# Kernel optimization log

Measured on AMD Instinct MI355X. Metric: run time of the kernel, lower is better.

The kernel has to match this reference:

```python
import jax, jax.numpy as jnp
import numpy as np

NODE_CARDS = [119, 5, 12, 12, 10, 6, 6, 2, 2]
EDGE_CARDS = [5, 6, 2]
HIDDEN = 256
LAYERS = 5
N = 60000
E = 180000
G = 2048  # num graphs (fixed num_segments)
BN_EPS = 1e-5

_NODE_OFFS = np.concatenate([[0], np.cumsum(NODE_CARDS[:-1])]).astype(np.int32)
_EDGE_OFFS = np.concatenate([[0], np.cumsum(EDGE_CARDS[:-1])]).astype(np.int32)
_NODE_MAX = np.asarray(NODE_CARDS, np.int32) - 1
_EDGE_MAX = np.asarray(EDGE_CARDS, np.int32) - 1


def _cat_sum(x, table, maxs, offs):
    # x: [N, F] int; table: [sum(cards), H] -> [N, H]
    idx = jnp.clip(x, 0, maxs[None, :]) + offs[None, :]
    return table[idx].sum(axis=1)


def setup_inputs() -> dict:
    key = jax.random.key(0)
    ks = jax.random.split(key, 32)
    w = 0.0625  # ~ xavier for 256

    def nrm(k, shape, s=w):
        return jax.random.normal(k, shape, dtype=jnp.float32) * s

    inp = {
        'x': jax.random.randint(ks[0], (N, len(NODE_CARDS)), 0, 119, dtype=jnp.int32),
        'edge_index': jax.random.randint(ks[1], (2, E), 0, N, dtype=jnp.int32),
        'edge_attr': jax.random.randint(ks[2], (E, len(EDGE_CARDS)), 0, 6, dtype=jnp.int32),
        'batch': jnp.sort(jax.random.randint(ks[3], (N,), 0, G, dtype=jnp.int32)),
        # embeddings
        'node_emb': nrm(ks[4], (int(sum(NODE_CARDS)), HIDDEN), 0.1),
        'edge_emb': nrm(ks[5], (int(sum(EDGE_CARDS)), HIDDEN), 0.1),
        'vn_emb': nrm(ks[6], (1, HIDDEN), 0.1),
        # GINE conv: eps + 2-layer MLP per layer (stacked)
        'eps': jnp.zeros((LAYERS,), jnp.float32),
        'W1': nrm(ks[7], (LAYERS, HIDDEN, HIDDEN)),
        'b1': jnp.zeros((LAYERS, HIDDEN), jnp.float32),
        'W2': nrm(ks[8], (LAYERS, HIDDEN, HIDDEN)),
        'b2': jnp.zeros((LAYERS, HIDDEN), jnp.float32),
        # BatchNorm (eval mode: running stats)
        'bn_gamma': jnp.ones((LAYERS, HIDDEN), jnp.float32),
        'bn_beta': jnp.zeros((LAYERS, HIDDEN), jnp.float32),
        'bn_mean': nrm(ks[9], (LAYERS, HIDDEN), 0.02),
        'bn_var': jnp.ones((LAYERS, HIDDEN), jnp.float32),
        # virtual-node MLP per layer
        'vW1': nrm(ks[10], (LAYERS, HIDDEN, HIDDEN)),
        'vb1': jnp.zeros((LAYERS, HIDDEN), jnp.float32),
        'vW2': nrm(ks[11], (LAYERS, HIDDEN, HIDDEN)),
        'vb2': jnp.zeros((LAYERS, HIDDEN), jnp.float32),
        # head MLP (2 layers: hidden->hidden->1)
        'hW1': nrm(ks[12], (HIDDEN, HIDDEN)),
        'hb1': jnp.zeros((HIDDEN,), jnp.float32),
        'hW2': nrm(ks[13], (HIDDEN, 1)),
        'hb2': jnp.zeros((1,), jnp.float32),
    }
    return inp


def reference(x, edge_index, edge_attr, batch,
              node_emb, edge_emb, vn_emb, eps,
              W1, b1, W2, b2,
              bn_gamma, bn_beta, bn_mean, bn_var,
              vW1, vb1, vW2, vb2,
              hW1, hb1, hW2, hb2):
    node_maxs = jnp.asarray(_NODE_MAX)
    node_offs = jnp.asarray(_NODE_OFFS)
    edge_maxs = jnp.asarray(_EDGE_MAX)
    edge_offs = jnp.asarray(_EDGE_OFFS)

    h = _cat_sum(x, node_emb, node_maxs, node_offs)          # [N, H]
    ea = _cat_sum(edge_attr, edge_emb, edge_maxs, edge_offs)  # [E, H]
    src, dst = edge_index[0], edge_index[1]

    vn = jnp.broadcast_to(vn_emb[0], (G, HIDDEN))  # [G, H]

    def mean_pool(h_):
        s = jax.ops.segment_sum(h_, batch, num_segments=G)
        cnt = jax.ops.segment_sum(jnp.ones((h_.shape[0], 1), h_.dtype), batch, num_segments=G)
        return s / jnp.maximum(cnt, 1.0)

    for l in range(LAYERS):
        h = h + vn[batch]
        # GINEConv: msg = relu(x_src + edge_attr); agg scatter-add onto dst
        msg = jax.nn.relu(h[src] + ea)                        # [E, H]
        agg = jax.ops.segment_sum(msg, dst, num_segments=N)   # [N, H]
        z = (1.0 + eps[l]) * h + agg
        z = jax.nn.relu(z @ W1[l] + b1[l]) @ W2[l] + b2[l]
        # BatchNorm1d (eval, running stats)
        z = (z - bn_mean[l]) * (bn_gamma[l] / jnp.sqrt(bn_var[l] + BN_EPS)) + bn_beta[l]
        h = jax.nn.relu(z)
        # virtual-node update
        g = mean_pool(h)
        vn = vn + (jax.nn.relu(g @ vW1[l] + vb1[l]) @ vW2[l] + vb2[l])

    g = mean_pool(h)                                          # [G, H]
    logits = (jax.nn.relu(g @ hW1 + hb1) @ hW2 + hb2).reshape(-1)  # [G]
    return logits
```

## Files before the change

kernel.cpp:

```cpp
#include <hip/hip_runtime.h>

#define NN 60000
#define NE 180000
#define NG 2048
#define NL 5
#define CAP 32

typedef unsigned short u16;
typedef unsigned int u32;
typedef __bf16 bf16x8 __attribute__((ext_vector_type(8)));
typedef float f32x4 __attribute__((ext_vector_type(4)));

__device__ __forceinline__ u16 f2bf(float f) {
    u32 u = __builtin_bit_cast(u32, f);
    u += 0x7FFFu + ((u >> 16) & 1u);
    return (u16)(u >> 16);
}
__device__ __forceinline__ float bf2f(u16 s) {
    return __builtin_bit_cast(float, (u32)s << 16);
}
__device__ __forceinline__ float bflo(u32 w) {
    return __builtin_bit_cast(float, w << 16);
}
__device__ __forceinline__ float bfhi(u32 w) {
    return __builtin_bit_cast(float, w & 0xFFFF0000u);
}
__device__ __forceinline__ u32 pack2bf(float lo, float hi) {
    return (u32)f2bf(lo) | ((u32)f2bf(hi) << 16);
}
__device__ __forceinline__ void gload_lds16(const void* g, void* l) {
    __builtin_amdgcn_global_load_lds(
        (const __attribute__((address_space(1))) unsigned int*)g,
        (__attribute__((address_space(3))) unsigned int*)l, 16, 0, 0);
}
__device__ __forceinline__ int swz(int row, int col) {
    return (row << 9) + ((((col >> 3) ^ (row & 7))) << 4) + ((col & 7) << 1);
}

__constant__ int NODE_OFF[9]  = {0, 119, 124, 136, 148, 158, 164, 170, 172};
__constant__ int NODE_MAXC[9] = {118, 4, 11, 11, 9, 5, 5, 1, 1};

__global__ __launch_bounds__(256) void k_prep_weights(
    const float* __restrict__ W1, const float* __restrict__ W2,
    const float* __restrict__ vW1, const float* __restrict__ vW2,
    const float* __restrict__ hW1, u16* __restrict__ Wt)
{
    int mat = blockIdx.x >> 8;
    int n = blockIdx.x & 255;
    int k = threadIdx.x;
    const float* src;
    if (mat < 5)       src = W1 + (size_t)mat * 65536;
    else if (mat < 10) src = W2 + (size_t)(mat - 5) * 65536;
    else if (mat < 15) src = vW1 + (size_t)(mat - 10) * 65536;
    else if (mat < 20) src = vW2 + (size_t)(mat - 15) * 65536;
    else               src = hW1;
    Wt[(size_t)mat * 65536 + n * 256 + k] = f2bf(src[k * 256 + n]);
}

__global__ __launch_bounds__(256) void k_misc(
    const float* __restrict__ eemb, const int* __restrict__ batch,
    const float* __restrict__ vn_emb,
    u16* __restrict__ comb, int* __restrict__ starts,
    float* __restrict__ vn, u16* __restrict__ vnbf, float* __restrict__ gsum)
{
    int b = blockIdx.x;
    if (b < 2048) {
        int i = b * 256 + threadIdx.x;
        float v = vn_emb[i & 255];
        vn[i] = v;
        vnbf[i] = f2bf(v);
        gsum[i] = 0.f;
    } else if (b < 2108) {
        int r = b - 2048, c = threadIdx.x;
        int a0 = r / 12, a1 = (r % 12) / 2, a2 = r & 1;
        comb[r * 256 + c] = f2bf(eemb[a0 * 256 + c] + eemb[(5 + a1) * 256 + c] +
                                 eemb[(11 + a2) * 256 + c]);
    } else {
        int g = (b - 2108) * 256 + threadIdx.x;
        if (g > NG) return;
        int lo = 0, hi = NN;
        while (lo < hi) {
            int mid = (lo + hi) >> 1;
            if (batch[mid] < g) lo = mid + 1; else hi = mid;
        }
        starts[g] = lo;
    }
}

__global__ __launch_bounds__(256) void k_embed(const int* __restrict__ x,
                                               const float* __restrict__ node_emb,
                                               u16* __restrict__ hbf,
                                               int* __restrict__ deg)
{
    int i = blockIdx.x * 4 + (threadIdx.x >> 6);
    if (i >= NN) return;
    if ((threadIdx.x & 63) == 0) deg[i] = 0;
    int c = (threadIdx.x & 63) * 4;
    float4 s = make_float4(0.f, 0.f, 0.f, 0.f);
#pragma unroll
    for (int f = 0; f < 9; ++f) {
        int xv = x[i * 9 + f];
        xv = xv < 0 ? 0 : (xv > NODE_MAXC[f] ? NODE_MAXC[f] : xv);
        const float4 t = *(const float4*)&node_emb[(size_t)(NODE_OFF[f] + xv) * 256 + c];
        s.x += t.x; s.y += t.y; s.z += t.z; s.w += t.w;
    }
    ushort4 o;
    o.x = f2bf(s.x); o.y = f2bf(s.y); o.z = f2bf(s.z); o.w = f2bf(s.w);
    *(ushort4*)&hbf[(size_t)i * 256 + c] = o;
}

__global__ __launch_bounds__(256) void k_bucket(
    const int* __restrict__ src, const int* __restrict__ dst,
    const int* __restrict__ eattr, int* __restrict__ deg, u32* __restrict__ slots)
{
    int e = blockIdx.x * 256 + threadIdx.x;
    if (e >= NE) return;
    int a0 = eattr[e * 3 + 0]; a0 = a0 < 0 ? 0 : (a0 > 4 ? 4 : a0);
    int a1 = eattr[e * 3 + 1]; a1 = a1 < 0 ? 0 : (a1 > 5 ? 5 : a1);
    int a2 = eattr[e * 3 + 2]; a2 = a2 < 0 ? 0 : (a2 > 1 ? 1 : a2);
    u32 code = (u32)(a0 * 12 + a1 * 2 + a2);
    int d = dst[e];
    int p = atomicAdd(&deg[d], 1);
    if (p < CAP) slots[(size_t)d * CAP + p] = (u32)src[e] | (code << 17);
}

__global__ __launch_bounds__(256) void k_agg(
    const u16* __restrict__ hbf, const u16* __restrict__ vnbf,
    const int* __restrict__ batch, const u32* __restrict__ slots,
    const int* __restrict__ deg, const u16* __restrict__ comb,
    u16* __restrict__ Abf, const float* __restrict__ epsp)
{
    const int wid = threadIdx.x >> 6, lane = threadIdx.x & 63;
    const int half = lane >> 5, l32 = lane & 31;
    const int d = blockIdx.x * 8 + wid * 2 + half;
    const int c = l32 * 8;
    int nd = deg[d];
    nd = nd > CAP ? CAP : nd;

    const u32* sl = slots + (size_t)d * CAP;
    u32 sv_l = (l32 < nd) ? sl[l32] : 0u;
    int b_l = (l32 < nd) ? batch[sv_l & 0x1FFFFu] : 0;

    float acc[8] = {0.f, 0.f, 0.f, 0.f, 0.f, 0.f, 0.f, 0.f};
    for (int p = 0; p < nd; ++p) {
        int srcl = (lane & 32) | p;
        u32 sv = (u32)__shfl((int)sv_l, srcl);
        int b  = __shfl(b_l, srcl);
        int s  = (int)(sv & 0x1FFFFu);
        int code = (int)(sv >> 17);
        const uint4 hv = *(const uint4*)&hbf[(size_t)s * 256 + c];
        const uint4 vv = *(const uint4*)&vnbf[(size_t)b * 256 + c];
        const uint4 tv = *(const uint4*)&comb[(size_t)code * 256 + c];
        const u32* hw = (const u32*)&hv;
        const u32* vw = (const u32*)&vv;
        const u32* tw = (const u32*)&tv;
#pragma unroll
        for (int e = 0; e < 4; ++e) {
            acc[e * 2 + 0] += fmaxf(bflo(hw[e]) + bflo(vw[e]) + bflo(tw[e]), 0.f);
            acc[e * 2 + 1] += fmaxf(bfhi(hw[e]) + bfhi(vw[e]) + bfhi(tw[e]), 0.f);
        }
    }

    int bd = batch[d];
    float ep = 1.0f + *epsp;
    const uint4 hd = *(const uint4*)&hbf[(size_t)d * 256 + c];
    const uint4 vd = *(const uint4*)&vnbf[(size_t)bd * 256 + c];
    const u32* hw = (const u32*)&hd;
    const u32* vw = (const u32*)&vd;
    uint4 o;
    u32* op = (u32*)&o;
#pragma unroll
    for (int e = 0; e < 4; ++e) {
        float lo = (bflo(hw[e]) + bflo(vw[e])) * ep + acc[e * 2 + 0];
        float hi = (bfhi(hw[e]) + bfhi(vw[e])) * ep + acc[e * 2 + 1];
        op[e] = pack2bf(lo, hi);
    }
    *(uint4*)&Abf[(size_t)d * 256 + c] = o;
}

__device__ __forceinline__ void loadW(bf16x8 (&B)[2][4], const u16* __restrict__ W,
                                      int hk, int wn, int cl, int rg)
{
#pragma unroll
    for (int j = 0; j < 2; ++j) {
        const char* p = (const char*)W + (size_t)(wn + j * 16 + cl) * 512 + hk * 256 + (rg << 4);
#pragma unroll
        for (int ks = 0; ks < 4; ++ks)
            B[j][ks] = __builtin_bit_cast(bf16x8, *(const uint4*)(p + ks * 64));
    }
}

__device__ __forceinline__ void gemmHalf(f32x4 (&acc)[4][2], const bf16x8 (&B)[2][4],
                                         const u16* Tl, int hk, int cl, int rg)
{
#pragma unroll
    for (int ks = 0; ks < 4; ++ks) {
#pragma unroll
        for (int i = 0; i < 4; ++i) {
            int ar = i * 16 + cl;
            int ch = hk * 16 + ks * 4 + rg;
            bf16x8 af = __builtin_bit_cast(bf16x8,
                *(const uint4*)((const char*)Tl + (ar << 9) + ((ch ^ (ar & 7)) << 4)));
            acc[i][0] = __builtin_amdgcn_mfma_f32_16x16x32_bf16(af, B[0][ks], acc[i][0], 0, 0, 0);
            acc[i][1] = __builtin_amdgcn_mfma_f32_16x16x32_bf16(af, B[1][ks], acc[i][1], 0, 0, 0);
        }
    }
}

__global__ __launch_bounds__(512) void k_mlp3(
    const u16* __restrict__ Abf, u16* __restrict__ hnxt,
    const int* __restrict__ batch,
    const u16* __restrict__ W1t, const u16* __restrict__ W2t,
    const float* __restrict__ b1, const float* __restrict__ b2,
    const float* __restrict__ bng, const float* __restrict__ bnb,
    const float* __restrict__ bnm, const float* __restrict__ bnv,
    float* __restrict__ gsum)
{
    __shared__ __align__(16) u16 Tl[64 * 256];
    __shared__ int batchLds[64];
    const int m0 = blockIdx.x * 64;
    const int tid = threadIdx.x, lane = tid & 63, wid = tid >> 6;
    const int wn = wid * 32;
    const int cl = lane & 15, rg = lane >> 4;

    if (tid < 64) batchLds[tid] = (m0 + tid < NN) ? batch[m0 + tid] : -1;

    bf16x8 Ba[2][4], Bb[2][4];
    loadW(Ba, W1t, 0, wn, cl, rg);

#pragma unroll
    for (int i = 0; i < 4; ++i) {
        int slot = i * 512 + tid;
        int row = slot >> 5, cch = slot & 31;
        int g = cch ^ (row & 7);
        gload_lds16((const char*)Abf + (size_t)(m0 + row) * 512 + (g << 4),
                    (char*)Tl + ((i * 512 + wid * 64) << 4));
    }
    loadW(Bb, W1t, 1, wn, cl, rg);

    __syncthreads();

    f32x4 acc1[4][2] = {};
    gemmHalf(acc1, Ba, Tl, 0, cl, rg);
    loadW(Ba, W2t, 0, wn, cl, rg);
    gemmHalf(acc1, Bb, Tl, 1, cl, rg);
    loadW(Bb, W2t, 1, wn, cl, rg);
    __syncthreads();

#pragma unroll
    for (int j = 0; j < 2; ++j) {
        int col = wn + j * 16 + cl;
        float bv = b1[col];
#pragma unroll
        for (int i = 0; i < 4; ++i)
#pragma unroll
            for (int r = 0; r < 4; ++r) {
                int row = i * 16 + rg * 4 + r;
                float v = fmaxf(acc1[i][j][r] + bv, 0.f);
                *(u16*)((char*)Tl + swz(row, col)) = f2bf(v);
            }
    }
    __syncthreads();

    f32x4 acc2[4][2] = {};
    gemmHalf(acc2, Ba, Tl, 0, cl, rg);
    gemmHalf(acc2, Bb, Tl, 1, cl, rg);

#pragma unroll
    for (int j = 0; j < 2; ++j) {
        int gn = wn + j * 16 + cl;
        float bv = b2[gn];
        float sc = bng[gn] * rsqrtf(bnv[gn] + 1e-5f);
        float sh = bnb[gn] - bnm[gn] * sc;
        float s = 0.f;
        int gcur = -1;
#pragma unroll
        for (int i = 0; i < 4; ++i) {
#pragma unroll
            for (int r = 0; r < 4; ++r) {
                int row = i * 16 + rg * 4 + r;
                int g = batchLds[row];
                float v = acc2[i][j][r] + bv;
                u16 hb = f2bf(fmaxf(v * sc + sh, 0.f));
                if (g >= 0) hnxt[(size_t)(m0 + row) * 256 + gn] = hb;
                if (g != gcur) {
                    if (gcur >= 0) atomicAdd(&gsum[(size_t)gcur * 256 + gn], s);
                    gcur = g; s = 0.f;
                }
                if (g >= 0) s += bf2f(hb);
            }
        }
        if (gcur >= 0) atomicAdd(&gsum[(size_t)gcur * 256 + gn], s);
    }
}

__device__ __forceinline__ void stageW(const u16* __restrict__ W, u16* Bl,
                                       int k0, int tid, int wid)
{
#pragma unroll
    for (int i = 0; i < 4; ++i) {
        int slot = i * 512 + tid;
        int row = slot >> 3, cch = slot & 7;
        int g = cch ^ (row & 7);
        gload_lds16((const char*)W + (size_t)row * 512 + (size_t)k0 * 2 + (g << 4),
                    (char*)Bl + ((i * 512 + wid * 64) << 4));
    }
}

__device__ __forceinline__ void gemm64(const u16* Tl, u16* Bl, const u16* __restrict__ W,
                                       f32x4 (&acc)[2][4], int wm, int wn,
                                       int lane, int tid, int wid)
{
    const int cl = lane & 15;
    for (int k0 = 0; k0 < 256; k0 += 64) {
        __syncthreads();
        stageW(W, Bl, k0, tid, wid);
        __syncthreads();
#pragma unroll
        for (int kw = 0; kw < 2; ++kw) {
            int q = kw * 4 + (lane >> 4);
            int qt = (k0 >> 3) + q;
            bf16x8 af[2], bfr[4];
#pragma unroll
            for (int t = 0; t < 2; ++t) {
                int ar = wm + t * 16 + cl;
                af[t] = __builtin_bit_cast(bf16x8,
                    *(const uint4*)((const char*)Tl + (ar << 9) + ((qt ^ (ar & 7)) << 4)));
            }
#pragma unroll
            for (int t = 0; t < 4; ++t) {
                int br = wn + t * 16 + cl;
                bfr[t] = __builtin_bit_cast(bf16x8,
                    *(const uint4*)((const char*)Bl + (br << 7) + ((q ^ (br & 7)) << 4)));
            }
#pragma unroll
            for (int i = 0; i < 2; ++i)
#pragma unroll
                for (int j = 0; j < 4; ++j)
                    acc[i][j] = __builtin_amdgcn_mfma_f32_16x16x32_bf16(af[i], bfr[j], acc[i][j], 0, 0, 0);
        }
    }
}

__device__ __forceinline__ void writeT(u16* Tl, const f32x4 (&acc)[2][4],
                                       const float* __restrict__ b1,
                                       int wm, int wn, int lane)
{
    const int cl = lane & 15, rg = lane >> 4;
#pragma unroll
    for (int j = 0; j < 4; ++j) {
        int col = wn + j * 16 + cl;
        float bv = b1[col];
#pragma unroll
        for (int i = 0; i < 2; ++i)
#pragma unroll
            for (int r = 0; r < 4; ++r) {
                int row = wm + i * 16 + rg * 4 + r;
                float v = fmaxf(acc[i][j][r] + bv, 0.f);
                *(u16*)((char*)Tl + swz(row, col)) = f2bf(v);
            }
    }
}

__global__ __launch_bounds__(512) void k_vnmlp(
    float* __restrict__ gsum, const int* __restrict__ starts,
    const u16* __restrict__ W1t, const u16* __restrict__ W2t,
    const float* __restrict__ b1, const float* __restrict__ b2,
    float* __restrict__ vn, u16* __restrict__ vnbf)
{
    __shared__ __align__(16) u16 Bl[256 * 64];
    __shared__ __align__(16) u16 Tl[64 * 256];
    const int m0 = blockIdx.x * 64;
    const int tid = threadIdx.x, lane = tid & 63, wid = tid >> 6;
    const int wm = (wid >> 2) * 32, wn = (wid & 3) * 64;
    const int cl = lane & 15, rg = lane >> 4;

    {
        const int c = lane * 4;
#pragma unroll
        for (int n = 0; n < 8; ++n) {
            int row = wid * 8 + n;
            int g = m0 + row;
            float4 sv = *(const float4*)&gsum[(size_t)g * 256 + c];
            *(float4*)&gsum[(size_t)g * 256 + c] = make_float4(0.f, 0.f, 0.f, 0.f);
            float cnt = (float)(starts[g + 1] - starts[g]);
            float inv = 1.0f / fmaxf(cnt, 1.0f);
            ushort4 o;
            o.x = f2bf(sv.x * inv); o.y = f2bf(sv.y * inv);
            o.z = f2bf(sv.z * inv); o.w = f2bf(sv.w * inv);
            *(ushort4*)((char*)Tl + swz(row, c)) = o;
        }
    }
    __syncthreads();

    f32x4 acc1[2][4] = {};
    gemm64(Tl, Bl, W1t, acc1, wm, wn, lane, tid, wid);
    __syncthreads();
    writeT(Tl, acc1, b1, wm, wn, lane);

    f32x4 acc2[2][4] = {};
    gemm64(Tl, Bl, W2t, acc2, wm, wn, lane, tid, wid);

#pragma unroll
    for (int j = 0; j < 4; ++j) {
        int gn = wn + j * 16 + cl;
        float bv = b2[gn];
#pragma unroll
        for (int i = 0; i < 2; ++i) {
#pragma unroll
            for (int r = 0; r < 4; ++r) {
                int gm = m0 + wm + i * 16 + rg * 4 + r;
                size_t idx = (size_t)gm * 256 + gn;
                float nv = vn[idx] + acc2[i][j][r] + bv;
                vn[idx] = nv;
                vnbf[idx] = f2bf(nv);
            }
        }
    }
}

__global__ __launch_bounds__(512) void k_headf(
    const float* __restrict__ gsum, const int* __restrict__ starts,
    const u16* __restrict__ W1t, const float* __restrict__ b1,
    const float* __restrict__ hW2, const float* __restrict__ hb2,
    float* __restrict__ out)
{
    __shared__ __align__(16) u16 Bl[256 * 64];
    __shared__ __align__(16) u16 Tl[64 * 256];
    const int m0 = blockIdx.x * 64;
    const int tid = threadIdx.x, lane = tid & 63, wid = tid >> 6;
    const int wm = (wid >> 2) * 32, wn = (wid & 3) * 64;

    {
        const int c = lane * 4;
#pragma unroll
        for (int n = 0; n < 8; ++n) {
            int row = wid * 8 + n;
            int g = m0 + row;
            float4 sv = *(const float4*)&gsum[(size_t)g * 256 + c];
            float cnt = (float)(starts[g + 1] - starts[g]);
            float inv = 1.0f / fmaxf(cnt, 1.0f);
            ushort4 o;
            o.x = f2bf(sv.x * inv); o.y = f2bf(sv.y * inv);
            o.z = f2bf(sv.z * inv); o.w = f2bf(sv.w * inv);
            *(ushort4*)((char*)Tl + swz(row, c)) = o;
        }
    }
    __syncthreads();

    f32x4 acc1[2][4] = {};
    gemm64(Tl, Bl, W1t, acc1, wm, wn, lane, tid, wid);
    __syncthreads();
    writeT(Tl, acc1, b1, wm, wn, lane);
    __syncthreads();

    int row = tid >> 3, oct = tid & 7;
    float s = 0.f;
#pragma unroll
    for (int c = 0; c < 32; ++c) {
        int col = oct * 32 + c;
        s += bf2f(*(const u16*)((const char*)Tl + swz(row, col))) * hW2[col];
    }
    s += __shfl_down(s, 4);
    s += __shfl_down(s, 2);
    s += __shfl_down(s, 1);
    if (oct == 0) out[m0 + row] = s + hb2[0];
}

extern "C" void kernel_launch(void* const* d_in, const int* in_sizes, int n_in,
                              void* d_out, int out_size, void* d_ws, size_t ws_size,
                              hipStream_t stream)
{
    const int*   x        = (const int*)d_in[0];
    const int*   ei       = (const int*)d_in[1];
    const int*   eattr    = (const int*)d_in[2];
    const int*   batch    = (const int*)d_in[3];
    const float* node_emb = (const float*)d_in[4];
    const float* edge_emb = (const float*)d_in[5];
    const float* vn_emb   = (const float*)d_in[6];
    const float* eps      = (const float*)d_in[7];
    const float* W1       = (const float*)d_in[8];
    const float* b1       = (const float*)d_in[9];
    const float* W2       = (const float*)d_in[10];
    const float* b2       = (const float*)d_in[11];
    const float* bng      = (const float*)d_in[12];
    const float* bnb      = (const float*)d_in[13];
    const float* bnm      = (const float*)d_in[14];
    const float* bnv      = (const float*)d_in[15];
    const float* vW1      = (const float*)d_in[16];
    const float* vb1      = (const float*)d_in[17];
    const float* vW2      = (const float*)d_in[18];
    const float* vb2      = (const float*)d_in[19];
    const float* hW1      = (const float*)d_in[20];
    const float* hb1      = (const float*)d_in[21];
    const float* hW2      = (const float*)d_in[22];
    const float* hb2      = (const float*)d_in[23];
    float* out = (float*)d_out;

    char* ws = (char*)d_ws;
    size_t off = 0;
    auto alloc = [&](size_t b) {
        char* p = ws + off;
        off = (off + b + 255) & ~(size_t)255;
        return p;
    };
    u16*   hbf0 = (u16*)alloc((size_t)NN * 256 * 2);
    u16*   hbf1 = (u16*)alloc((size_t)NN * 256 * 2);
    u16*   Abf  = (u16*)alloc((size_t)NN * 256 * 2 + 65536);
    float* vn   = (float*)alloc((size_t)NG * 256 * 4);
    u16*   vnbf = (u16*)alloc((size_t)NG * 256 * 2);
    float* gsum = (float*)alloc((size_t)NG * 256 * 4);
    u16*   Wt   = (u16*)alloc((size_t)21 * 65536 * 2);
    int*   starts = (int*)alloc((size_t)(NG + 1) * 4);
    u16*   comb = (u16*)alloc((size_t)60 * 256 * 2);
    int*   deg  = (int*)alloc((size_t)NN * 4);
    u32*   slots = (u32*)alloc((size_t)NN * CAP * 4);

    const int* srcI = ei;
    const int* dstI = ei + NE;

    k_prep_weights<<<21 * 256, 256, 0, stream>>>(W1, W2, vW1, vW2, hW1, Wt);
    k_misc<<<2117, 256, 0, stream>>>(edge_emb, batch, vn_emb, comb, starts, vn, vnbf, gsum);
    k_embed<<<NN / 4, 256, 0, stream>>>(x, node_emb, hbf0, deg);
    k_bucket<<<(NE + 255) / 256, 256, 0, stream>>>(srcI, dstI, eattr, deg, slots);

    const int GBIG = (NN + 63) / 64;
    const int GSM  = NG / 64;

    u16* hcur = hbf0;
    u16* hnxt = hbf1;
    for (int l = 0; l < NL; ++l) {
        k_agg<<<NN / 8, 256, 0, stream>>>(hcur, vnbf, batch, slots, deg, comb, Abf, eps + l);
        k_mlp3<<<GBIG, 512, 0, stream>>>(Abf, hnxt, batch,
                                         Wt + (size_t)(0 + l) * 65536,
                                         Wt + (size_t)(5 + l) * 65536,
                                         b1 + l * 256, b2 + l * 256,
                                         bng + l * 256, bnb + l * 256,
                                         bnm + l * 256, bnv + l * 256,
                                         gsum);
        if (l < NL - 1) {
            k_vnmlp<<<GSM, 512, 0, stream>>>(gsum, starts,
                                             Wt + (size_t)(10 + l) * 65536,
                                             Wt + (size_t)(15 + l) * 65536,
                                             vb1 + l * 256, vb2 + l * 256,
                                             vn, vnbf);
        }
        u16* t = hcur; hcur = hnxt; hnxt = t;
    }
    k_headf<<<GSM, 512, 0, stream>>>(gsum, starts, Wt + (size_t)20 * 65536,
                                     hb1, hW2, hb2, out);
}
```

Measured before the change: 545.5 us.

## Stage MLP weights through double-buffered LDS with 2x4 warp tiling

The fused node MLP kernel now streams both weight matrices through a double-buffered LDS tile in 32-wide K chunks with a swizzled layout, instead of each wave loading its weight columns straight from global memory into registers. Waves are rearranged into a 2x4 grid of 32x64 output tiles, so each wave's A and B fragment loads feed more MFMAs. This cuts register pressure from holding full weight fragments and overlaps the next chunk's global load with the current MFMAs. The cost is extra LDS (64KB total per block, which may limit occupancy) and sixteen block-wide barriers per kernel.

```diff
diff --git a/kernel.cpp b/kernel.cpp
--- a/kernel.cpp
+++ b/kernel.cpp
@@ -35,6 +35,9 @@
 }
 __device__ __forceinline__ int swz(int row, int col) {
     return (row << 9) + ((((col >> 3) ^ (row & 7))) << 4) + ((col & 7) << 1);
+}
+__device__ __forceinline__ int bswz(int row) {
+    return (row & 3) ^ ((row >> 2) & 3);
 }
 
 __constant__ int NODE_OFF[9]  = {0, 119, 124, 136, 148, 158, 164, 170, 172};
@@ -178,36 +181,65 @@
     *(uint4*)&Abf[(size_t)d * 256 + c] = o;
 }
 
-__device__ __forceinline__ void loadW(bf16x8 (&B)[2][4], const u16* __restrict__ W,
-                                      int hk, int wn, int cl, int rg)
-{
-#pragma unroll
-    for (int j = 0; j < 2; ++j) {
-        const char* p = (const char*)W + (size_t)(wn + j * 16 + cl) * 512 + hk * 256 + (rg << 4);
-#pragma unroll
-        for (int ks = 0; ks < 4; ++ks)
-            B[j][ks] = __builtin_bit_cast(bf16x8, *(const uint4*)(p + ks * 64));
-    }
-}
-
-__device__ __forceinline__ void gemmHalf(f32x4 (&acc)[4][2], const bf16x8 (&B)[2][4],
-                                         const u16* Tl, int hk, int cl, int rg)
-{
-#pragma unroll
-    for (int ks = 0; ks < 4; ++ks) {
-#pragma unroll
-        for (int i = 0; i < 4; ++i) {
-            int ar = i * 16 + cl;
-            int ch = hk * 16 + ks * 4 + rg;
-            bf16x8 af = __builtin_bit_cast(bf16x8,
-                *(const uint4*)((const char*)Tl + (ar << 9) + ((ch ^ (ar & 7)) << 4)));
-            acc[i][0] = __builtin_amdgcn_mfma_f32_16x16x32_bf16(af, B[0][ks], acc[i][0], 0, 0, 0);
-            acc[i][1] = __builtin_amdgcn_mfma_f32_16x16x32_bf16(af, B[1][ks], acc[i][1], 0, 0, 0);
-        }
-    }
-}
-
-__global__ __launch_bounds__(512) void k_mlp3(
+__device__ __forceinline__ void stageW32(const u16* __restrict__ W, u16* Bp,
+                                         int k0, int tid, int wid)
+{
+#pragma unroll
+    for (int i = 0; i < 2; ++i) {
+        int slot = i * 512 + tid;
+        int row = slot >> 2, cch = slot & 3;
+        int g = cch ^ bswz(row);
+        gload_lds16((const char*)W + (size_t)row * 512 + (size_t)k0 * 2 + (g << 4),
+                    (char*)Bp + ((i * 512 + wid * 64) << 4));
+    }
+}
+
+__device__ __forceinline__ void gemmPhase32(const u16* Tl, const u16* Bp,
+                                            f32x4 (&acc)[2][4], int p,
+                                            int wm, int wn, int cl, int rg)
+{
+    bf16x8 af[2], bfr[4];
+    int ch = p * 4 + rg;
+#pragma unroll
+    for (int t = 0; t < 2; ++t) {
+        int ar = wm + t * 16 + cl;
+        af[t] = __builtin_bit_cast(bf16x8,
+            *(const uint4*)((const char*)Tl + (ar << 9) + ((ch ^ (ar & 7)) << 4)));
+    }
+#pragma unroll
+    for (int u = 0; u < 4; ++u) {
+        int br = wn + u * 16 + cl;
+        bfr[u] = __builtin_bit_cast(bf16x8,
+            *(const uint4*)((const char*)Bp + (br << 6) + ((rg ^ bswz(br)) << 4)));
+    }
+#pragma unroll
+    for (int t = 0; t < 2; ++t)
+#pragma unroll
+        for (int u = 0; u < 4; ++u)
+            acc[t][u] = __builtin_amdgcn_mfma_f32_16x16x32_bf16(af[t], bfr[u], acc[t][u], 0, 0, 0);
+}
+
+__device__ __forceinline__ void writeT(u16* Tl, const f32x4 (&acc)[2][4],
+                                       const float* __restrict__ b1,
+                                       int wm, int wn, int lane)
+{
+    const int cl = lane & 15, rg = lane >> 4;
+#pragma unroll
+    for (int j = 0; j < 4; ++j) {
+        int col = wn + j * 16 + cl;
+        float bv = b1[col];
+#pragma unroll
+        for (int i = 0; i < 2; ++i)
+#pragma unroll
+            for (int r = 0; r < 4; ++r) {
+                int row = wm + i * 16 + rg * 4 + r;
+                float v = fmaxf(acc[i][j][r] + bv, 0.f);
+                *(u16*)((char*)Tl + swz(row, col)) = f2bf(v);
+            }
+    }
+}
+
+__global__ __launch_bounds__(512) void k_mlpP2(
     const u16* __restrict__ Abf, u16* __restrict__ hnxt,
     const int* __restrict__ batch,
     const u16* __restrict__ W1t, const u16* __restrict__ W2t,
@@ -217,16 +249,14 @@
     float* __restrict__ gsum)
 {
     __shared__ __align__(16) u16 Tl[64 * 256];
+    __shared__ __align__(16) u16 Bl[2][256 * 32];
     __shared__ int batchLds[64];
     const int m0 = blockIdx.x * 64;
     const int tid = threadIdx.x, lane = tid & 63, wid = tid >> 6;
-    const int wn = wid * 32;
+    const int wm = (wid >> 2) * 32, wn = (wid & 3) * 64;
     const int cl = lane & 15, rg = lane >> 4;
 
     if (tid < 64) batchLds[tid] = (m0 + tid < NN) ? batch[m0 + tid] : -1;
-
-    bf16x8 Ba[2][4], Bb[2][4];
-    loadW(Ba, W1t, 0, wn, cl, rg);
 
 #pragma unroll
     for (int i = 0; i < 4; ++i) {
@@ -236,38 +266,31 @@
         gload_lds16((const char*)Abf + (size_t)(m0 + row) * 512 + (g << 4),
                     (char*)Tl + ((i * 512 + wid * 64) << 4));
     }
-    loadW(Bb, W1t, 1, wn, cl, rg);
-
-    __syncthreads();
-
-    f32x4 acc1[4][2] = {};
-    gemmHalf(acc1, Ba, Tl, 0, cl, rg);
-    loadW(Ba, W2t, 0, wn, cl, rg);
-    gemmHalf(acc1, Bb, Tl, 1, cl, rg);
-    loadW(Bb, W2t, 1, wn, cl, rg);
-    __syncthreads();
-
-#pragma unroll
-    for (int j = 0; j < 2; ++j) {
-        int col = wn + j * 16 + cl;
-        float bv = b1[col];
-#pragma unroll
-        for (int i = 0; i < 4; ++i)
-#pragma unroll
-            for (int r = 0; r < 4; ++r) {
-                int row = i * 16 + rg * 4 + r;
-                float v = fmaxf(acc1[i][j][r] + bv, 0.f);
-                *(u16*)((char*)Tl + swz(row, col)) = f2bf(v);
-            }
-    }
-    __syncthreads();
-
-    f32x4 acc2[4][2] = {};
-    gemmHalf(acc2, Ba, Tl, 0, cl, rg);
-    gemmHalf(acc2, Bb, Tl, 1, cl, rg);
-
-#pragma unroll
-    for (int j = 0; j < 2; ++j) {
+    stageW32(W1t, Bl[0], 0, tid, wid);
+    __syncthreads();
+
+    f32x4 acc1[2][4] = {};
+#pragma unroll
+    for (int p = 0; p < 8; ++p) {
+        if (p < 7) stageW32(W1t, Bl[(p + 1) & 1], (p + 1) * 32, tid, wid);
+        else       stageW32(W2t, Bl[0], 0, tid, wid);
+        gemmPhase32(Tl, Bl[p & 1], acc1, p, wm, wn, cl, rg);
+        __syncthreads();
+    }
+
+    writeT(Tl, acc1, b1, wm, wn, lane);
+    __syncthreads();
+
+    f32x4 acc2[2][4] = {};
+#pragma unroll
+    for (int p = 0; p < 8; ++p) {
+        if (p < 7) stageW32(W2t, Bl[(p + 1) & 1], (p + 1) * 32, tid, wid);
+        gemmPhase32(Tl, Bl[p & 1], acc2, p, wm, wn, cl, rg);
+        __syncthreads();
+    }
+
+#pragma unroll
+    for (int j = 0; j < 4; ++j) {
         int gn = wn + j * 16 + cl;
         float bv = b2[gn];
         float sc = bng[gn] * rsqrtf(bnv[gn] + 1e-5f);
@@ -275,10 +298,10 @@
         float s = 0.f;
         int gcur = -1;
 #pragma unroll
-        for (int i = 0; i < 4; ++i) {
+        for (int i = 0; i < 2; ++i) {
 #pragma unroll
             for (int r = 0; r < 4; ++r) {
-                int row = i * 16 + rg * 4 + r;
+                int row = wm + i * 16 + rg * 4 + r;
                 int g = batchLds[row];
                 float v = acc2[i][j][r] + bv;
                 u16 hb = f2bf(fmaxf(v * sc + sh, 0.f));
@@ -339,26 +362,6 @@
                 for (int j = 0; j < 4; ++j)
                     acc[i][j] = __builtin_amdgcn_mfma_f32_16x16x32_bf16(af[i], bfr[j], acc[i][j], 0, 0, 0);
         }
-    }
-}
-
-__device__ __forceinline__ void writeT(u16* Tl, const f32x4 (&acc)[2][4],
-                                       const float* __restrict__ b1,
-                                       int wm, int wn, int lane)
-{
-    const int cl = lane & 15, rg = lane >> 4;
-#pragma unroll
-    for (int j = 0; j < 4; ++j) {
-        int col = wn + j * 16 + cl;
-        float bv = b1[col];
-#pragma unroll
-        for (int i = 0; i < 2; ++i)
-#pragma unroll
-            for (int r = 0; r < 4; ++r) {
-                int row = wm + i * 16 + rg * 4 + r;
-                float v = fmaxf(acc[i][j][r] + bv, 0.f);
-                *(u16*)((char*)Tl + swz(row, col)) = f2bf(v);
-            }
     }
 }
 
@@ -531,13 +534,13 @@
     u16* hnxt = hbf1;
     for (int l = 0; l < NL; ++l) {
         k_agg<<<NN / 8, 256, 0, stream>>>(hcur, vnbf, batch, slots, deg, comb, Abf, eps + l);
-        k_mlp3<<<GBIG, 512, 0, stream>>>(Abf, hnxt, batch,
-                                         Wt + (size_t)(0 + l) * 65536,
-                                         Wt + (size_t)(5 + l) * 65536,
-                                         b1 + l * 256, b2 + l * 256,
-                                         bng + l * 256, bnb + l * 256,
-                                         bnm + l * 256, bnv + l * 256,
-                                         gsum);
+        k_mlpP2<<<GBIG, 512, 0, stream>>>(Abf, hnxt, batch,
+                                          Wt + (size_t)(0 + l) * 65536,
+                                          Wt + (size_t)(5 + l) * 65536,
+                                          b1 + l * 256, b2 + l * 256,
+                                          bng + l * 256, bnb + l * 256,
+                                          bnm + l * 256, bnv + l * 256,
+                                          gsum);
         if (l < NL - 1) {
             k_vnmlp<<<GSM, 512, 0, stream>>>(gsum, starts,
                                              Wt + (size_t)(10 + l) * 65536,
```

Result: no change. 546.2 us (+0.1%).
